# Kernel optimization log

Hardware: AMD Instinct MI355X
Metric: run time of the kernel (lower is better)

The kernel has to match this reference:

```python
import jax, jax.numpy as jnp
import numpy as np

NG, G = 256, 32          # num groups, pedestrians per group
E, H, MID, BN_EPS = 64, 64, 512, 1e-5
BOT = 32

def _bn(x, gamma, beta):
    # training-mode BatchNorm1d applied PER GROUP (axis=1 are the rows of
    # that group's pairwise batch), biased variance, eps=1e-5
    mean = jnp.mean(x, axis=1, keepdims=True)
    var = jnp.mean((x - mean) ** 2, axis=1, keepdims=True)
    return gamma * (x - mean) * jax.lax.rsqrt(var + BN_EPS) + beta

def setup_inputs() -> dict:
    key = jax.random.key(0)
    ks = jax.random.split(key, 8)
    B = NG * G
    starts = np.arange(NG, dtype=np.int64) * G
    seq_start_end = jnp.asarray(np.stack([starts, starts + G], axis=1))
    def lin(k, fi, fo):
        kw, kb = jax.random.split(k)
        lim = 1.0 / np.sqrt(fi)
        return (jax.random.uniform(kw, (fi, fo), jnp.float32, -lim, lim),
                jax.random.uniform(kb, (fo,), jnp.float32, -lim, lim))
    W_spatial, b_spatial = lin(ks[0], 2, E)
    W1, b1 = lin(ks[1], E + H, MID)
    W2, b2 = lin(ks[2], MID, BOT)
    return {
        'h_states': jax.random.normal(ks[3], (1, B, H), jnp.float32),
        'seq_start_end': seq_start_end,
        'end_pos': jax.random.normal(ks[4], (B, 2), jnp.float32),
        'W_spatial': W_spatial, 'b_spatial': b_spatial,
        'W1': W1, 'b1': b1,
        'gamma1': jnp.ones((MID,), jnp.float32), 'beta1': jnp.zeros((MID,), jnp.float32),
        'W2': W2, 'b2': b2,
        'gamma2': jnp.ones((BOT,), jnp.float32), 'beta2': jnp.zeros((BOT,), jnp.float32),
    }

def reference(h_states, seq_start_end, end_pos, W_spatial, b_spatial,
              W1, b1, gamma1, beta1, W2, b2, gamma2, beta2):
    B = end_pos.shape[0]
    ng = seq_start_end.shape[0]
    g = B // ng  # equal-size groups -> fully vectorized
    h = h_states.reshape(B, H).reshape(ng, g, H)
    pos = end_pos.reshape(ng, g, 2)
    # rel[n, i, j] = pos[n, j] - pos[n, i]  (matches repeat/tile in torch code)
    rel = pos[:, None, :, :] - pos[:, :, None, :]            # (ng, g, g, 2)
    emb = rel @ W_spatial + b_spatial                         # (ng, g, g, E)
    hb = jnp.broadcast_to(h[:, None, :, :], (ng, g, g, H))    # hidden of ped j
    x = jnp.concatenate([emb, hb], axis=-1).reshape(ng, g * g, E + H)
    x = jax.nn.relu(_bn(x @ W1 + b1, gamma1, beta1))          # (ng, g*g, 512)
    x = jax.nn.relu(_bn(x @ W2 + b2, gamma2, beta2))          # (ng, g*g, 32)
    pool = x.reshape(ng, g, g, BOT).max(axis=2)               # max over j
    return pool.reshape(B, BOT)
```

## Files before the change

### kernel.cpp

```cpp
#include <hip/hip_runtime.h>

#define GRP 32
#define HD 64
#define MIDD 512
#define LDSTR 520

typedef _Float16 half8 __attribute__((ext_vector_type(8)));
typedef float floatx4 __attribute__((ext_vector_type(4)));

__device__ inline half8 relu8(half8 x) {
    return __builtin_elementwise_max(x, (half8)(_Float16)0);
}

__launch_bounds__(512, 2)
__global__ void pool_all(const float* __restrict__ h_states,
                         const float* __restrict__ end_pos,
                         const float* __restrict__ Ws,
                         const float* __restrict__ W1,
                         const float* __restrict__ gamma1,
                         const float* __restrict__ beta1,
                         const float* __restrict__ W2,
                         const float* __restrict__ gamma2,
                         const float* __restrict__ beta2,
                         float* __restrict__ out) {
    __shared__ _Float16 Ash[32][LDSTR];
    __shared__ _Float16 Bsh[32][LDSTR];
    __shared__ _Float16 w2T[32][LDSTR];
    __shared__ float posx[32], posy[32];
    __shared__ float wr0s[512], wr1s[512];
    __shared__ float red[8][2][16][2];
    __shared__ float bns[32], bno[32];

    const int tid  = threadIdx.x;
    const int wave = tid >> 6;
    const int lane = tid & 63;
    const int quad = lane >> 4;
    const int n16  = lane & 15;
    const int g0   = blockIdx.x * GRP;

    if (tid < 32) {
        posx[tid] = end_pos[(g0 + tid) * 2];
        posy[tid] = end_pos[(g0 + tid) * 2 + 1];
    }
    {
        const int c = tid;
        float a0 = 0.f, a1 = 0.f;
#pragma unroll
        for (int e = 0; e < 64; ++e) {
            float w = W1[e * MIDD + c];
            a0 = fmaf(Ws[e], w, a0);
            a1 = fmaf(Ws[64 + e], w, a1);
        }
        wr0s[c] = a0;
        wr1s[c] = a1;
    }
#pragma unroll
    for (int it = 0; it < 32; ++it) {
        int idx = tid + it * 512;
        int k = idx >> 5, nn = idx & 31;
        w2T[nn][k] = (_Float16)W2[idx];
    }
    __syncthreads();

    {
        half8 afr[2][2];
#pragma unroll
        for (int mt = 0; mt < 2; ++mt)
#pragma unroll
            for (int kk = 0; kk < 2; ++kk) {
                const float4* hp = (const float4*)(h_states + (size_t)(g0 + mt * 16 + n16) * HD + kk * 32 + quad * 8);
                float4 p0 = hp[0], p1 = hp[1];
                half8 a;
                a[0] = (_Float16)p0.x; a[1] = (_Float16)p0.y; a[2] = (_Float16)p0.z; a[3] = (_Float16)p0.w;
                a[4] = (_Float16)p1.x; a[5] = (_Float16)p1.y; a[6] = (_Float16)p1.z; a[7] = (_Float16)p1.w;
                afr[mt][kk] = a;
            }

        floatx4 acc[2][4];
#pragma unroll
        for (int a = 0; a < 2; ++a)
#pragma unroll
            for (int b = 0; b < 4; ++b) acc[a][b] = (floatx4){0.f, 0.f, 0.f, 0.f};

#pragma unroll
        for (int nt4 = 0; nt4 < 4; ++nt4) {
            const int c = (wave * 4 + nt4) * 16 + n16;
#pragma unroll
            for (int kk = 0; kk < 2; ++kk) {
                half8 b;
#pragma unroll
                for (int x = 0; x < 8; ++x) {
                    int k = kk * 32 + quad * 8 + x;
                    b[x] = (_Float16)W1[(size_t)(64 + k) * MIDD + c];
                }
#pragma unroll
                for (int mt = 0; mt < 2; ++mt)
                    acc[mt][nt4] = __builtin_amdgcn_mfma_f32_16x16x32_f16(afr[mt][kk], b, acc[mt][nt4], 0, 0, 0);
            }
        }

#pragma unroll
        for (int nt4 = 0; nt4 < 4; ++nt4) {
            const int c = (wave * 4 + nt4) * 16 + n16;
            const float w0 = wr0s[c], w1 = wr1s[c];

            float su = 0.f, ssu = 0.f;
#pragma unroll
            for (int mt = 0; mt < 2; ++mt)
#pragma unroll
                for (int r = 0; r < 4; ++r) {
                    int j = mt * 16 + quad * 4 + r;
                    float u = acc[mt][nt4][r] + posx[j] * w0 + posy[j] * w1;
                    acc[mt][nt4][r] = u;
                    su += u;
                    ssu = fmaf(u, u, ssu);
                }
            su  += __shfl_xor(su, 16);  su  += __shfl_xor(su, 32);
            ssu += __shfl_xor(ssu, 16); ssu += __shfl_xor(ssu, 32);

            float vv[8];
            float sv = 0.f, ssv = 0.f;
#pragma unroll
            for (int ii = 0; ii < 8; ++ii) {
                int i = quad * 8 + ii;
                float v = posx[i] * w0 + posy[i] * w1;
                vv[ii] = v;
                sv += v;
                ssv = fmaf(v, v, ssv);
            }
            sv  += __shfl_xor(sv, 16);  sv  += __shfl_xor(sv, 32);
            ssv += __shfl_xor(ssv, 16); ssv += __shfl_xor(ssv, 32);

            const float muu = su * (1.f / 32.f), muv = sv * (1.f / 32.f);
            const float var = (ssu * (1.f / 32.f) - muu * muu) + (ssv * (1.f / 32.f) - muv * muv);
            const float s    = gamma1[c] * rsqrtf(var + 1e-5f);
            const float boff = s * (muu - muv) - beta1[c];

#pragma unroll
            for (int mt = 0; mt < 2; ++mt)
#pragma unroll
                for (int r = 0; r < 4; ++r) {
                    int j = mt * 16 + quad * 4 + r;
                    Ash[j][c] = (_Float16)(s * acc[mt][nt4][r]);
                }
#pragma unroll
            for (int ii = 0; ii < 8; ++ii)
                Bsh[quad * 8 + ii][c] = (_Float16)fmaf(s, vv[ii], boff);
        }
    }
    __syncthreads();

    floatx4 acc2[8][2];
#pragma unroll
    for (int a = 0; a < 8; ++a)
#pragma unroll
        for (int b = 0; b < 2; ++b) acc2[a][b] = (floatx4){0.f, 0.f, 0.f, 0.f};

#pragma unroll 2
    for (int kk = 0; kk < 16; ++kk) {
        const int kb = kk * 32 + quad * 8;
        const half8 w2f0 = *(const half8*)&w2T[n16][kb];
        const half8 w2f1 = *(const half8*)&w2T[16 + n16][kb];
        const half8 a0 = *(const half8*)&Ash[n16][kb];
        const half8 a1 = *(const half8*)&Ash[16 + n16][kb];
#pragma unroll
        for (int mp = 0; mp < 4; ++mp) {
            const int i = wave * 4 + mp;
            const half8 bf = *(const half8*)&Bsh[i][kb];
            const half8 z0 = relu8(a0 - bf);
            const half8 z1 = relu8(a1 - bf);
            acc2[2 * mp][0]     = __builtin_amdgcn_mfma_f32_16x16x32_f16(z0, w2f0, acc2[2 * mp][0], 0, 0, 0);
            acc2[2 * mp][1]     = __builtin_amdgcn_mfma_f32_16x16x32_f16(z0, w2f1, acc2[2 * mp][1], 0, 0, 0);
            acc2[2 * mp + 1][0] = __builtin_amdgcn_mfma_f32_16x16x32_f16(z1, w2f0, acc2[2 * mp + 1][0], 0, 0, 0);
            acc2[2 * mp + 1][1] = __builtin_amdgcn_mfma_f32_16x16x32_f16(z1, w2f1, acc2[2 * mp + 1][1], 0, 0, 0);
        }
    }

    float s0 = 0.f, q0 = 0.f, s1 = 0.f, q1 = 0.f;
#pragma unroll
    for (int mt = 0; mt < 8; ++mt)
#pragma unroll
        for (int r = 0; r < 4; ++r) {
            float v0 = acc2[mt][0][r], v1 = acc2[mt][1][r];
            s0 += v0; q0 = fmaf(v0, v0, q0);
            s1 += v1; q1 = fmaf(v1, v1, q1);
        }
    s0 += __shfl_xor(s0, 16); s0 += __shfl_xor(s0, 32);
    q0 += __shfl_xor(q0, 16); q0 += __shfl_xor(q0, 32);
    s1 += __shfl_xor(s1, 16); s1 += __shfl_xor(s1, 32);
    q1 += __shfl_xor(q1, 16); q1 += __shfl_xor(q1, 32);
    if (lane < 16) {
        red[wave][0][lane][0] = s0; red[wave][0][lane][1] = q0;
        red[wave][1][lane][0] = s1; red[wave][1][lane][1] = q1;
    }
    __syncthreads();
    if (tid < 32) {
        const int nt = tid >> 4, n = tid & 15;
        float s = 0.f, q = 0.f;
#pragma unroll
        for (int w = 0; w < 8; ++w) { s += red[w][nt][n][0]; q += red[w][nt][n][1]; }
        const float mu  = s * (1.f / 1024.f);
        const float var = q * (1.f / 1024.f) - mu * mu;
        const float sc  = gamma2[tid] * rsqrtf(var + 1e-5f);
        bns[tid] = sc;
        bno[tid] = beta2[tid] - sc * mu;
    }
    __syncthreads();

#pragma unroll
    for (int nt = 0; nt < 2; ++nt) {
        const int c = nt * 16 + n16;
        const float sc = bns[c], off = bno[c];
#pragma unroll
        for (int a = 0; a < 4; ++a) {
            float m = 0.f;
#pragma unroll
            for (int p = 0; p < 2; ++p)
#pragma unroll
                for (int r = 0; r < 4; ++r)
                    m = fmaxf(m, fmaf(sc, acc2[2 * a + p][nt][r], off));
            m = fmaxf(m, __shfl_xor(m, 16));
            m = fmaxf(m, __shfl_xor(m, 32));
            if (quad == nt) {
                const int i = wave * 4 + a;
                out[(size_t)(g0 + i) * 32 + c] = m;
            }
        }
    }
}

extern "C" void kernel_launch(void* const* d_in, const int* in_sizes, int n_in,
                              void* d_out, int out_size, void* d_ws, size_t ws_size,
                              hipStream_t stream) {
    (void)in_sizes; (void)n_in; (void)out_size; (void)d_ws; (void)ws_size;
    const float* h_states  = (const float*)d_in[0];
    const float* end_pos   = (const float*)d_in[2];
    const float* W_spatial = (const float*)d_in[3];
    const float* W1        = (const float*)d_in[5];
    const float* gamma1    = (const float*)d_in[7];
    const float* beta1     = (const float*)d_in[8];
    const float* W2        = (const float*)d_in[9];
    const float* gamma2    = (const float*)d_in[11];
    const float* beta2     = (const float*)d_in[12];
    float* out = (float*)d_out;

    pool_all<<<dim3(256), dim3(512), 0, stream>>>(h_states, end_pos, W_spatial, W1,
                                                  gamma1, beta1, W2, gamma2, beta2, out);
}
```

Baseline: 97.45 us.

## Overlap prologue loads with first GEMM and double-buffer LDS fragments in second GEMM

The h_states fragment loads and the W1 B-fragment loads and first MFMA GEMM now run before the first barrier, so they overlap with the Ws·W1 reduction and the W2 transpose instead of waiting on them. The Ws·W1 reduction uses four partial accumulators to shorten the dependency chain, and W2 is read as float4. The second GEMM loop is fully unrolled with register double-buffering of the LDS fragments, prefetching step k+1 while step k's MFMAs execute. The cost is higher register pressure, which could hurt occupancy under the 512x2 launch bounds.

```diff
diff --git a/kernel.cpp b/kernel.cpp
--- a/kernel.cpp
+++ b/kernel.cpp
@@ -42,111 +42,131 @@
         posx[tid] = end_pos[(g0 + tid) * 2];
         posy[tid] = end_pos[(g0 + tid) * 2 + 1];
     }
+
+    half8 afr[2][2];
+#pragma unroll
+    for (int mt = 0; mt < 2; ++mt)
+#pragma unroll
+        for (int kk = 0; kk < 2; ++kk) {
+            const float4* hp = (const float4*)(h_states + (size_t)(g0 + mt * 16 + n16) * HD + kk * 32 + quad * 8);
+            float4 p0 = hp[0], p1 = hp[1];
+            half8 a;
+            a[0] = (_Float16)p0.x; a[1] = (_Float16)p0.y; a[2] = (_Float16)p0.z; a[3] = (_Float16)p0.w;
+            a[4] = (_Float16)p1.x; a[5] = (_Float16)p1.y; a[6] = (_Float16)p1.z; a[7] = (_Float16)p1.w;
+            afr[mt][kk] = a;
+        }
+
     {
         const int c = tid;
-        float a0 = 0.f, a1 = 0.f;
-#pragma unroll
-        for (int e = 0; e < 64; ++e) {
-            float w = W1[e * MIDD + c];
-            a0 = fmaf(Ws[e], w, a0);
-            a1 = fmaf(Ws[64 + e], w, a1);
-        }
-        wr0s[c] = a0;
-        wr1s[c] = a1;
-    }
-#pragma unroll
-    for (int it = 0; it < 32; ++it) {
-        int idx = tid + it * 512;
-        int k = idx >> 5, nn = idx & 31;
-        w2T[nn][k] = (_Float16)W2[idx];
-    }
-    __syncthreads();
-
-    {
-        half8 afr[2][2];
+        float p0[4] = {0.f, 0.f, 0.f, 0.f}, p1[4] = {0.f, 0.f, 0.f, 0.f};
+#pragma unroll
+        for (int e = 0; e < 64; e += 4) {
+#pragma unroll
+            for (int u = 0; u < 4; ++u) {
+                float w = W1[(e + u) * MIDD + c];
+                p0[u] = fmaf(Ws[e + u], w, p0[u]);
+                p1[u] = fmaf(Ws[64 + e + u], w, p1[u]);
+            }
+        }
+        wr0s[c] = (p0[0] + p0[1]) + (p0[2] + p0[3]);
+        wr1s[c] = (p1[0] + p1[1]) + (p1[2] + p1[3]);
+    }
+
+    {
+        const float4* W2v = (const float4*)W2;
+#pragma unroll
+        for (int it = 0; it < 8; ++it) {
+            int i4 = tid + it * 512;
+            float4 p = W2v[i4];
+            int k = i4 >> 3, nn = (i4 & 7) * 4;
+            w2T[nn][k]     = (_Float16)p.x;
+            w2T[nn + 1][k] = (_Float16)p.y;
+            w2T[nn + 2][k] = (_Float16)p.z;
+            w2T[nn + 3][k] = (_Float16)p.w;
+        }
+    }
+
+    floatx4 acc[2][4];
+#pragma unroll
+    for (int a = 0; a < 2; ++a)
+#pragma unroll
+        for (int b = 0; b < 4; ++b) acc[a][b] = (floatx4){0.f, 0.f, 0.f, 0.f};
+
+    half8 bfr[4][2];
+#pragma unroll
+    for (int nt4 = 0; nt4 < 4; ++nt4) {
+        const int c = (wave * 4 + nt4) * 16 + n16;
+#pragma unroll
+        for (int kk = 0; kk < 2; ++kk) {
+            float t[8];
+#pragma unroll
+            for (int x = 0; x < 8; ++x) {
+                int k = kk * 32 + quad * 8 + x;
+                t[x] = W1[(size_t)(64 + k) * MIDD + c];
+            }
+            half8 b;
+#pragma unroll
+            for (int x = 0; x < 8; ++x) b[x] = (_Float16)t[x];
+            bfr[nt4][kk] = b;
+        }
+    }
+#pragma unroll
+    for (int nt4 = 0; nt4 < 4; ++nt4)
+#pragma unroll
+        for (int kk = 0; kk < 2; ++kk)
+#pragma unroll
+            for (int mt = 0; mt < 2; ++mt)
+                acc[mt][nt4] = __builtin_amdgcn_mfma_f32_16x16x32_f16(afr[mt][kk], bfr[nt4][kk], acc[mt][nt4], 0, 0, 0);
+
+    __syncthreads();
+
+#pragma unroll
+    for (int nt4 = 0; nt4 < 4; ++nt4) {
+        const int c = (wave * 4 + nt4) * 16 + n16;
+        const float w0 = wr0s[c], w1 = wr1s[c];
+
+        float su = 0.f, ssu = 0.f;
 #pragma unroll
         for (int mt = 0; mt < 2; ++mt)
 #pragma unroll
-            for (int kk = 0; kk < 2; ++kk) {
-                const float4* hp = (const float4*)(h_states + (size_t)(g0 + mt * 16 + n16) * HD + kk * 32 + quad * 8);
-                float4 p0 = hp[0], p1 = hp[1];
-                half8 a;
-                a[0] = (_Float16)p0.x; a[1] = (_Float16)p0.y; a[2] = (_Float16)p0.z; a[3] = (_Float16)p0.w;
-                a[4] = (_Float16)p1.x; a[5] = (_Float16)p1.y; a[6] = (_Float16)p1.z; a[7] = (_Float16)p1.w;
-                afr[mt][kk] = a;
-            }
-
-        floatx4 acc[2][4];
-#pragma unroll
-        for (int a = 0; a < 2; ++a)
-#pragma unroll
-            for (int b = 0; b < 4; ++b) acc[a][b] = (floatx4){0.f, 0.f, 0.f, 0.f};
-
-#pragma unroll
-        for (int nt4 = 0; nt4 < 4; ++nt4) {
-            const int c = (wave * 4 + nt4) * 16 + n16;
-#pragma unroll
-            for (int kk = 0; kk < 2; ++kk) {
-                half8 b;
-#pragma unroll
-                for (int x = 0; x < 8; ++x) {
-                    int k = kk * 32 + quad * 8 + x;
-                    b[x] = (_Float16)W1[(size_t)(64 + k) * MIDD + c];
-                }
-#pragma unroll
-                for (int mt = 0; mt < 2; ++mt)
-                    acc[mt][nt4] = __builtin_amdgcn_mfma_f32_16x16x32_f16(afr[mt][kk], b, acc[mt][nt4], 0, 0, 0);
-            }
-        }
-
-#pragma unroll
-        for (int nt4 = 0; nt4 < 4; ++nt4) {
-            const int c = (wave * 4 + nt4) * 16 + n16;
-            const float w0 = wr0s[c], w1 = wr1s[c];
-
-            float su = 0.f, ssu = 0.f;
-#pragma unroll
-            for (int mt = 0; mt < 2; ++mt)
-#pragma unroll
-                for (int r = 0; r < 4; ++r) {
-                    int j = mt * 16 + quad * 4 + r;
-                    float u = acc[mt][nt4][r] + posx[j] * w0 + posy[j] * w1;
-                    acc[mt][nt4][r] = u;
-                    su += u;
-                    ssu = fmaf(u, u, ssu);
-                }
-            su  += __shfl_xor(su, 16);  su  += __shfl_xor(su, 32);
-            ssu += __shfl_xor(ssu, 16); ssu += __shfl_xor(ssu, 32);
-
-            float vv[8];
-            float sv = 0.f, ssv = 0.f;
-#pragma unroll
-            for (int ii = 0; ii < 8; ++ii) {
-                int i = quad * 8 + ii;
-                float v = posx[i] * w0 + posy[i] * w1;
-                vv[ii] = v;
-                sv += v;
-                ssv = fmaf(v, v, ssv);
-            }
-            sv  += __shfl_xor(sv, 16);  sv  += __shfl_xor(sv, 32);
-            ssv += __shfl_xor(ssv, 16); ssv += __shfl_xor(ssv, 32);
-
-            const float muu = su * (1.f / 32.f), muv = sv * (1.f / 32.f);
-            const float var = (ssu * (1.f / 32.f) - muu * muu) + (ssv * (1.f / 32.f) - muv * muv);
-            const float s    = gamma1[c] * rsqrtf(var + 1e-5f);
-            const float boff = s * (muu - muv) - beta1[c];
-
-#pragma unroll
-            for (int mt = 0; mt < 2; ++mt)
-#pragma unroll
-                for (int r = 0; r < 4; ++r) {
-                    int j = mt * 16 + quad * 4 + r;
-                    Ash[j][c] = (_Float16)(s * acc[mt][nt4][r]);
-                }
-#pragma unroll
-            for (int ii = 0; ii < 8; ++ii)
-                Bsh[quad * 8 + ii][c] = (_Float16)fmaf(s, vv[ii], boff);
-        }
+            for (int r = 0; r < 4; ++r) {
+                int j = mt * 16 + quad * 4 + r;
+                float u = acc[mt][nt4][r] + posx[j] * w0 + posy[j] * w1;
+                acc[mt][nt4][r] = u;
+                su += u;
+                ssu = fmaf(u, u, ssu);
+            }
+        su  += __shfl_xor(su, 16);  su  += __shfl_xor(su, 32);
+        ssu += __shfl_xor(ssu, 16); ssu += __shfl_xor(ssu, 32);
+
+        float vv[8];
+        float sv = 0.f, ssv = 0.f;
+#pragma unroll
+        for (int ii = 0; ii < 8; ++ii) {
+            int i = quad * 8 + ii;
+            float v = posx[i] * w0 + posy[i] * w1;
+            vv[ii] = v;
+            sv += v;
+            ssv = fmaf(v, v, ssv);
+        }
+        sv  += __shfl_xor(sv, 16);  sv  += __shfl_xor(sv, 32);
+        ssv += __shfl_xor(ssv, 16); ssv += __shfl_xor(ssv, 32);
+
+        const float muu = su * (1.f / 32.f), muv = sv * (1.f / 32.f);
+        const float var = (ssu * (1.f / 32.f) - muu * muu) + (ssv * (1.f / 32.f) - muv * muv);
+        const float s    = gamma1[c] * rsqrtf(var + 1e-5f);
+        const float boff = s * (muu - muv) - beta1[c];
+
+#pragma unroll
+        for (int mt = 0; mt < 2; ++mt)
+#pragma unroll
+            for (int r = 0; r < 4; ++r) {
+                int j = mt * 16 + quad * 4 + r;
+                Ash[j][c] = (_Float16)(s * acc[mt][nt4][r]);
+            }
+#pragma unroll
+        for (int ii = 0; ii < 8; ++ii)
+            Bsh[quad * 8 + ii][c] = (_Float16)fmaf(s, vv[ii], boff);
     }
     __syncthreads();
 
@@ -156,23 +176,50 @@
 #pragma unroll
         for (int b = 0; b < 2; ++b) acc2[a][b] = (floatx4){0.f, 0.f, 0.f, 0.f};
 
-#pragma unroll 2
-    for (int kk = 0; kk < 16; ++kk) {
-        const int kb = kk * 32 + quad * 8;
-        const half8 w2f0 = *(const half8*)&w2T[n16][kb];
-        const half8 w2f1 = *(const half8*)&w2T[16 + n16][kb];
-        const half8 a0 = *(const half8*)&Ash[n16][kb];
-        const half8 a1 = *(const half8*)&Ash[16 + n16][kb];
+    const int ib = wave * 4;
+    half8 pa0[2], pa1[2], pw0[2], pw1[2], pbf[2][4];
+    {
+        const int kb = quad * 8;
+        pw0[0] = *(const half8*)&w2T[n16][kb];
+        pw1[0] = *(const half8*)&w2T[16 + n16][kb];
+        pa0[0] = *(const half8*)&Ash[n16][kb];
+        pa1[0] = *(const half8*)&Ash[16 + n16][kb];
+#pragma unroll
+        for (int mp = 0; mp < 4; ++mp) pbf[0][mp] = *(const half8*)&Bsh[ib + mp][kb];
+    }
+#pragma unroll
+    for (int kk = 0; kk < 15; ++kk) {
+        const int cur = kk & 1, nxt = cur ^ 1;
+        {
+            const int kb = (kk + 1) * 32 + quad * 8;
+            pw0[nxt] = *(const half8*)&w2T[n16][kb];
+            pw1[nxt] = *(const half8*)&w2T[16 + n16][kb];
+            pa0[nxt] = *(const half8*)&Ash[n16][kb];
+            pa1[nxt] = *(const half8*)&Ash[16 + n16][kb];
+#pragma unroll
+            for (int mp = 0; mp < 4; ++mp) pbf[nxt][mp] = *(const half8*)&Bsh[ib + mp][kb];
+        }
 #pragma unroll
         for (int mp = 0; mp < 4; ++mp) {
-            const int i = wave * 4 + mp;
-            const half8 bf = *(const half8*)&Bsh[i][kb];
-            const half8 z0 = relu8(a0 - bf);
-            const half8 z1 = relu8(a1 - bf);
-            acc2[2 * mp][0]     = __builtin_amdgcn_mfma_f32_16x16x32_f16(z0, w2f0, acc2[2 * mp][0], 0, 0, 0);
-            acc2[2 * mp][1]     = __builtin_amdgcn_mfma_f32_16x16x32_f16(z0, w2f1, acc2[2 * mp][1], 0, 0, 0);
-            acc2[2 * mp + 1][0] = __builtin_amdgcn_mfma_f32_16x16x32_f16(z1, w2f0, acc2[2 * mp + 1][0], 0, 0, 0);
-            acc2[2 * mp + 1][1] = __builtin_amdgcn_mfma_f32_16x16x32_f16(z1, w2f1, acc2[2 * mp + 1][1], 0, 0, 0);
+            const half8 bf = pbf[cur][mp];
+            const half8 z0 = relu8(pa0[cur] - bf);
+            const half8 z1 = relu8(pa1[cur] - bf);
+            acc2[2 * mp][0]     = __builtin_amdgcn_mfma_f32_16x16x32_f16(z0, pw0[cur], acc2[2 * mp][0], 0, 0, 0);
+            acc2[2 * mp][1]     = __builtin_amdgcn_mfma_f32_16x16x32_f16(z0, pw1[cur], acc2[2 * mp][1], 0, 0, 0);
+            acc2[2 * mp + 1][0] = __builtin_amdgcn_mfma_f32_16x16x32_f16(z1, pw0[cur], acc2[2 * mp + 1][0], 0, 0, 0);
+            acc2[2 * mp + 1][1] = __builtin_amdgcn_mfma_f32_16x16x32_f16(z1, pw1[cur], acc2[2 * mp + 1][1], 0, 0, 0);
+        }
+    }
+    {
+#pragma unroll
+        for (int mp = 0; mp < 4; ++mp) {
+            const half8 bf = pbf[1][mp];
+            const half8 z0 = relu8(pa0[1] - bf);
+            const half8 z1 = relu8(pa1[1] - bf);
+            acc2[2 * mp][0]     = __builtin_amdgcn_mfma_f32_16x16x32_f16(z0, pw0[1], acc2[2 * mp][0], 0, 0, 0);
+            acc2[2 * mp][1]     = __builtin_amdgcn_mfma_f32_16x16x32_f16(z0, pw1[1], acc2[2 * mp][1], 0, 0, 0);
+            acc2[2 * mp + 1][0] = __builtin_amdgcn_mfma_f32_16x16x32_f16(z1, pw0[1], acc2[2 * mp + 1][0], 0, 0, 0);
+            acc2[2 * mp + 1][1] = __builtin_amdgcn_mfma_f32_16x16x32_f16(z1, pw1[1], acc2[2 * mp + 1][1], 0, 0, 0);
         }
     }
 
```

Result: no change. 96.51 us, median of 2 (-1.0%).
